# Kernel tuning notes

Measured on AMD Instinct MI355X. Metric: run time of the kernel, lower is better.

Reference implementation:

```python
import jax, jax.numpy as jnp
import numpy as np

GAMMA = 0.03125  # 1/D
REG = 1e-3


def rbf_gram(X, Y, gamma):
    # avoiding the naive [N, M, D] diff tensor from the torch source.
    xx = jnp.sum(X * X, axis=-1)  # [N]
    yy = jnp.sum(Y * Y, axis=-1)  # [M]
    sq = xx[:, None] + yy[None, :] - 2.0 * (X @ Y.T)  # [N, M]
    sq = jnp.maximum(sq, 0.0)
    return jnp.exp(-gamma * sq)


def setup_inputs() -> dict:
    key = jax.random.key(0)
    k1, k2, k3 = jax.random.split(key, 3)
    N, M, D = 8192, 8192, 32
    X_train = jax.random.normal(k1, (N, D), dtype=jnp.float32)
    y_train = jax.random.normal(k2, (N,), dtype=jnp.float32)
    X_test = jax.random.normal(k3, (M, D), dtype=jnp.float32)
    return {"X_train": X_train, "y_train": y_train, "X_test": X_test}


def reference(X_train, y_train, X_test):
    # fit: solve (K + reg * I) alpha = y
    N = X_train.shape[0]
    K = rbf_gram(X_train, X_train, GAMMA)  # [N, N]
    A = K + REG * jnp.eye(N, dtype=K.dtype)
    alpha = jnp.linalg.solve(A, y_train[:, None])[:, 0]  # [N]
    # predict: K_test @ alpha
    K_test = rbf_gram(X_test, X_train, GAMMA)  # [M, N]
    return K_test @ alpha  # [M]
```

## Files before the change

### kernel.cpp

```cpp
#include <hip/hip_runtime.h>


#define NN 8192
#define DD 32
#define REGL 1e-3f
#define NITER 94
#define NBLK 256
#define NSL 16
#define NRB 16
#define ROWS 512
#define COLS 512
#define NC2 (-0.045084220027780106f)
#define SCF (0.3002806023f)

typedef short v8s __attribute__((ext_vector_type(8)));
typedef float v4f __attribute__((ext_vector_type(4)));

__device__ __forceinline__ float fast_exp2(float x) {
#if __has_builtin(__builtin_amdgcn_exp2f)
  return __builtin_amdgcn_exp2f(x);
#else
  float r;
  asm("v_exp_f32 %0, %1" : "=v"(r) : "v"(x));
  return r;
#endif
}

__device__ __forceinline__ float ld_f(const float* p) {
  return __hip_atomic_load(p, __ATOMIC_RELAXED, __HIP_MEMORY_SCOPE_AGENT);
}
__device__ __forceinline__ void st_f(float* p, float v) {
  __hip_atomic_store(p, v, __ATOMIC_RELAXED, __HIP_MEMORY_SCOPE_AGENT);
}
__device__ __forceinline__ double ld_d(const double* p) {
  return __hip_atomic_load(p, __ATOMIC_RELAXED, __HIP_MEMORY_SCOPE_AGENT);
}
__device__ __forceinline__ void st_d(double* p, double v) {
  __hip_atomic_store(p, v, __ATOMIC_RELAXED, __HIP_MEMORY_SCOPE_AGENT);
}

__device__ __forceinline__ ushort f2bf(float x) {
  unsigned u = __float_as_uint(x);
  return (ushort)((u + 0x7fff + ((u >> 16) & 1)) >> 16);
}
__device__ __forceinline__ float bf2f(ushort b) {
  return __uint_as_float(((unsigned)b) << 16);
}

__device__ __forceinline__ double bfly64_d(double v) {
#pragma unroll
  for (int m = 1; m < 64; m <<= 1) v += __shfl_xor(v, m, 64);
  return v;
}
__device__ __forceinline__ double wave_down_sum_d(double v) {
#pragma unroll
  for (int off = 32; off > 0; off >>= 1) v += __shfl_down(v, off, 64);
  return v;
}

__device__ __forceinline__ float gather16_pair(const float* qp, int rowpair,
                                               int e) {
  const double* qpd = (const double*)qp + (rowpair >> 1);
  float mine[8], recv[8];
#pragma unroll
  for (int k = 0; k < 8; ++k) {
    union {
      double d;
      float f[2];
    } u;
    u.d = ld_d(qpd + (size_t)(e * 8 + k) * (NN / 2));
    mine[k] = e ? u.f[1] : u.f[0];
    recv[k] = e ? u.f[0] : u.f[1];
  }
#pragma unroll
  for (int k = 0; k < 8; ++k) recv[k] = __shfl_xor(recv[k], 1, 64);
  float s = 0.f;
#pragma unroll
  for (int k = 0; k < 8; ++k) s += e ? recv[k] : mine[k];
#pragma unroll
  for (int k = 0; k < 8; ++k) s += e ? mine[k] : recv[k];
  return s;
}

__device__ __forceinline__ void gbarrier(unsigned* bar, int par) {
  __builtin_amdgcn_s_waitcnt(0);
  __syncthreads();
  if (threadIdx.x == 0) {
    unsigned* gen = bar + 272;
    unsigned* base = bar + (par << 9);
    unsigned g =
        __hip_atomic_load(gen, __ATOMIC_RELAXED, __HIP_MEMORY_SCOPE_AGENT);
    unsigned a = __hip_atomic_fetch_add(&base[(blockIdx.x >> 4) * 16], 1u,
                                        __ATOMIC_RELAXED,
                                        __HIP_MEMORY_SCOPE_AGENT);
    bool pub = false;
    if (a == 15u) {
      unsigned ra = __hip_atomic_fetch_add(base + 256, 1u, __ATOMIC_RELAXED,
                                           __HIP_MEMORY_SCOPE_AGENT);
      if (ra == 15u) {
        __hip_atomic_store(gen, g + 1u, __ATOMIC_RELAXED,
                           __HIP_MEMORY_SCOPE_AGENT);
        pub = true;
#pragma unroll
        for (int k = 0; k < 16; ++k)
          __hip_atomic_store(&base[k * 16], 0u, __ATOMIC_RELAXED,
                             __HIP_MEMORY_SCOPE_AGENT);
        __hip_atomic_store(base + 256, 0u, __ATOMIC_RELAXED,
                           __HIP_MEMORY_SCOPE_AGENT);
      }
    }
    if (!pub) {
      unsigned t = 0;
      while (__hip_atomic_load(gen, __ATOMIC_RELAXED,
                               __HIP_MEMORY_SCOPE_AGENT) == g) {
        if (t < 64)
          __builtin_amdgcn_s_sleep(1);
        else
          __builtin_amdgcn_s_sleep(8);
        if (++t > (1u << 20)) break;
      }
    }
  }
  __atomic_signal_fence(__ATOMIC_SEQ_CST);
  __syncthreads();
}

__device__ __forceinline__ void conv_frag(const float* __restrict__ X, int row,
                                          int kb, v8s& h, v8s& l) {
  const float4* rp = (const float4*)(X + (size_t)row * DD + kb);
  float4 f0 = rp[0], f1 = rp[1];
  float f[8] = {f0.x, f0.y, f0.z, f0.w, f1.x, f1.y, f1.z, f1.w};
  union {
    v8s v;
    ushort u[8];
  } H, L;
#pragma unroll
  for (int j = 0; j < 8; ++j) {
    float fs = SCF * f[j];
    ushort hb = f2bf(fs);
    H.u[j] = hb;
    L.u[j] = f2bf(fs - bf2f(hb));
  }
  h = H.v;
  l = L.v;
}


__global__ void setup_zero(unsigned* __restrict__ bar) {
  int i = blockIdx.x * 256 + threadIdx.x;
  if (i < 1024) bar[i] = 0u;
}

__global__ void row_norms(const float* __restrict__ X, float* __restrict__ xx) {
  int i = blockIdx.x * blockDim.x + threadIdx.x;
  if (i < NN) {
    const float4* row = (const float4*)(X + (size_t)i * DD);
    float s = 0.f;
#pragma unroll
    for (int k = 0; k < DD / 4; ++k) {
      float4 v = row[k];
      s += v.x * v.x + v.y * v.y + v.z * v.z + v.w * v.w;
    }
    xx[i] = NC2 * s;
  }
}

__device__ __forceinline__ void mv_compute(const v8s* ah, const v8s* al,
                                           const ushort (*Bh)[512],
                                           const ushort (*Bl)[512],
                                           const float* Wj, int lane,
                                           float racc[2][4]) {
  const int n = lane & 15;
  for (int t = 0; t < 32; ++t) {
    v8s bh = *(const v8s*)&Bh[t][lane * 8];
    v8s bl = *(const v8s*)&Bl[t][lane * 8];
    float wn = Wj[t * 16 + n];
#pragma unroll
    for (int rs = 0; rs < 2; ++rs) {
      v4f c = {0.f, 0.f, 0.f, 0.f};
      c = __builtin_amdgcn_mfma_f32_16x16x32_bf16(al[rs], bh, c, 0, 0, 0);
      c = __builtin_amdgcn_mfma_f32_16x16x32_bf16(ah[rs], bl, c, 0, 0, 0);
      c = __builtin_amdgcn_mfma_f32_16x16x32_bf16(ah[rs], bh, c, 0, 0, 0);
#pragma unroll
      for (int u = 0; u < 4; ++u)
        racc[rs][u] = fmaf(fast_exp2(c[u]), wn, racc[rs][u]);
    }
  }
}


__global__ __launch_bounds__(1024, 4) void cg_persist(
    const float* __restrict__ Xtr, const float* __restrict__ Xte,
    const float* __restrict__ xx_tr, const float* __restrict__ xx_te,
    const float* __restrict__ y, float* __restrict__ qp0,
    float* __restrict__ qp1, double* __restrict__ rho_s,
    double* __restrict__ mu_s, unsigned* __restrict__ bar,
    float* __restrict__ out, int db) {
  __shared__ __align__(16) ushort Bh[32][512];
  __shared__ __align__(16) ushort Bl[32][512];
  __shared__ float Wj[512];
  __shared__ float Ebj[512];
  __shared__ float Erow[512];
  __shared__ float Rrow[512], Qrow[512];
  __shared__ float Rcol[512], Qcol[512], Pcol[512], Xcol[512];
  __shared__ double sredq[16];
  __shared__ double sredr[16];
  __shared__ float s_ab[2];

  const int tid = threadIdx.x;
  const int lane = tid & 63;
  const int wid = tid >> 6;
  const int n = lane & 15, q4 = lane >> 4;
  const int rbi = blockIdx.x & 15;
  const int sli = blockIdx.x >> 4;
  const int rowbase = rbi * ROWS;
  const int i0 = rowbase + wid * 32;
  const int jbase = sli * COLS;

#pragma unroll
  for (int rep = 0; rep < 2; ++rep) {
    int idx = rep * 1024 + tid;
    int c = idx & 511;
    int g = idx >> 9;
    int j = jbase + c;
    const float4* rp = (const float4*)(Xtr + (size_t)j * DD + g * 8);
    float4 f0 = rp[0], f1 = rp[1];
    float f[8] = {f0.x, f0.y, f0.z, f0.w, f1.x, f1.y, f1.z, f1.w};
    union {
      ushort u[8];
      uint4 qq;
    } H, L;
#pragma unroll
    for (int e = 0; e < 8; ++e) {
      float fs = SCF * f[e];
      ushort hb = f2bf(fs);
      H.u[e] = hb;
      L.u[e] = f2bf(fs - bf2f(hb));
    }
    int tile = c >> 4, cl = c & 15;
    int ln = cl + 16 * g;
    *(uint4*)&Bh[tile][ln * 8] = H.qq;
    *(uint4*)&Bl[tile][ln * 8] = L.qq;
  }
  if (tid < 512) {
    Ebj[tid] = fast_exp2(xx_tr[jbase + tid]);
    Erow[tid] = fast_exp2(xx_tr[rowbase + tid]);
    Rrow[tid] = y[rowbase + tid];
    Qrow[tid] = 0.f;
    Rcol[tid] = y[jbase + tid];
    Qcol[tid] = 0.f;
    Pcol[tid] = 0.f;
    Xcol[tid] = 0.f;
  }

  v8s ah[2], al[2];
#pragma unroll
  for (int rs = 0; rs < 2; ++rs)
    conv_frag(Xtr, i0 + rs * 16 + n, q4 * 8, ah[rs], al[rs]);

  double rho_old = 1.0, alpha_old = 1.0;
  __syncthreads();

  for (int it = 0; it < NITER; ++it) {
    float* qp = (db && (it & 1)) ? qp1 : qp0;

    if (tid >= 512) {
      int ct = tid - 512;
      Wj[ct] = Rcol[ct] * Ebj[ct];
    }
    if (sli == 0) {
      float rvv = (tid < 512) ? Rrow[tid] : 0.f;
      double acc = wave_down_sum_d((double)rvv * (double)rvv);
      if (lane == 0) sredr[wid] = acc;
    }
    __syncthreads();
    if (sli == 0 && tid == 0) {
      double t = 0.0;
#pragma unroll
      for (int k3 = 0; k3 < 16; ++k3) t += sredr[k3];
      st_d(&rho_s[(size_t)it * 256 + rbi * 16], t);
    }

    float racc[2][4] = {};
    mv_compute(ah, al, Bh, Bl, Wj, lane, racc);
#pragma unroll
    for (int rs = 0; rs < 2; ++rs)
#pragma unroll
      for (int u = 0; u < 4; ++u) {
#pragma unroll
        for (int m = 1; m < 16; m <<= 1)
          racc[rs][u] += __shfl_xor(racc[rs][u], m, 64);
      }
    double cmu = 0.0;
    if (n == 0) {
#pragma unroll
      for (int rs = 0; rs < 2; ++rs)
#pragma unroll
        for (int u = 0; u < 4; ++u) {
          int lrow = wid * 32 + rs * 16 + q4 * 4 + u;
          float qc = racc[rs][u] * Erow[lrow];
          st_f(&qp[(size_t)sli * NN + rowbase + lrow], qc);
          cmu += (double)qc * (double)Rrow[lrow];
        }
    }
    cmu = bfly64_d(cmu);
    if (lane == 0) sredq[wid] = cmu;
    __syncthreads();
    if (tid == 0) {
      double t = 0.0;
#pragma unroll
      for (int k3 = 0; k3 < 16; ++k3) t += sredq[k3];
      st_d(&mu_s[(size_t)it * 256 + blockIdx.x], t);
    }

    gbarrier(bar, db ? (it & 1) : 0);

    if (wid == 0) {
      const double* mb = mu_s + (size_t)it * 256;
      double m = ld_d(mb + lane) + ld_d(mb + lane + 64) +
                 ld_d(mb + lane + 128) + ld_d(mb + lane + 192);
      double rv_l =
          (lane < 16) ? ld_d(rho_s + (size_t)it * 256 + lane * 16) : 0.0;
      double m1 = bfly64_d(m);
      double r1 = bfly64_d(rv_l);
      double mu = m1 + (double)REGL * r1;
      double beta_d = (it == 0) ? 0.0 : r1 / rho_old;
      double alpha_d =
          (it == 0) ? r1 / mu : r1 / (mu - r1 * beta_d / alpha_old);
      rho_old = r1;
      alpha_old = alpha_d;
      if (lane == 0) {
        s_ab[0] = (float)alpha_d;
        s_ab[1] = (float)beta_d;
      }
    }
    __syncthreads();
    const float alpha = s_ab[0], beta = s_ab[1];

    if (tid < 512) {
      float s = gather16_pair(qp, rowbase + (tid & ~1), tid & 1);
      float wr = fmaf(REGL, Rrow[tid], s);
      float qn = fmaf(beta, Qrow[tid], wr);
      Qrow[tid] = qn;
      Rrow[tid] = fmaf(-alpha, qn, Rrow[tid]);
    } else {
      int ct = tid - 512;
      float s = gather16_pair(qp, jbase + (ct & ~1), ct & 1);
      float wc = fmaf(REGL, Rcol[ct], s);
      float qn = fmaf(beta, Qcol[ct], wc);
      Qcol[ct] = qn;
      float pn = fmaf(beta, Pcol[ct], Rcol[ct]);
      Pcol[ct] = pn;
      Xcol[ct] = fmaf(alpha, pn, Xcol[ct]);
      Rcol[ct] = fmaf(-alpha, qn, Rcol[ct]);
    }
    if (!db) gbarrier(bar, 1);
  }

  {
    v8s th[2], tl[2];
#pragma unroll
    for (int rs = 0; rs < 2; ++rs)
      conv_frag(Xte, i0 + rs * 16 + n, q4 * 8, th[rs], tl[rs]);
    if (tid >= 512) {
      int ct = tid - 512;
      Wj[ct] = Xcol[ct] * Ebj[ct];
    } else {
      Erow[tid] = fast_exp2(xx_te[rowbase + tid]);
    }
    __syncthreads();
    float racc[2][4] = {};
    mv_compute(th, tl, Bh, Bl, Wj, lane, racc);
#pragma unroll
    for (int rs = 0; rs < 2; ++rs)
#pragma unroll
      for (int u = 0; u < 4; ++u) {
#pragma unroll
        for (int m = 1; m < 16; m <<= 1)
          racc[rs][u] += __shfl_xor(racc[rs][u], m, 64);
      }
    if (n == 0) {
#pragma unroll
      for (int rs = 0; rs < 2; ++rs)
#pragma unroll
        for (int u = 0; u < 4; ++u) {
          int lrow = wid * 32 + rs * 16 + q4 * 4 + u;
          st_f(&qp0[(size_t)sli * NN + rowbase + lrow],
               racc[rs][u] * Erow[lrow]);
        }
    }
    gbarrier(bar, 0);
    if (sli == 0 && tid < 512) {
      const float* qb = qp0 + rowbase + tid;
      float s = 0.f;
#pragma unroll
      for (int s2 = 0; s2 < NSL; ++s2) s += ld_f(qb + (size_t)s2 * NN);
      out[rowbase + tid] = s;
    }
  }
}


extern "C" void kernel_launch(void* const* d_in, const int* in_sizes, int n_in,
                              void* d_out, int out_size, void* d_ws,
                              size_t ws_size, hipStream_t stream) {
  const float* X_train = (const float*)d_in[0];
  const float* y_train = (const float*)d_in[1];
  const float* X_test = (const float*)d_in[2];
  float* out = (float*)d_out;

  char* w = (char*)d_ws;
  size_t off = 0;
  float* xx_tr = (float*)(w + off); off += NN * 4;
  float* xx_te = (float*)(w + off); off += NN * 4;
  double* rho_s = (double*)(w + off); off += (size_t)NITER * 256 * 8;
  double* mu_s = (double*)(w + off); off += (size_t)NITER * 256 * 8;
  unsigned* bar = (unsigned*)(w + off); off += 4096;
  off = (off + 255) & ~(size_t)255;
  float* qp0 = (float*)(w + off); off += (size_t)NSL * NN * 4;
  size_t need0 = off;
  float* qp1 = (float*)(w + off); off += (size_t)NSL * NN * 4;
  size_t need1 = off;

  int db = (ws_size >= need1) ? 1 : 0;
  if (ws_size < need0) return;
  if (!db) qp1 = qp0;

  setup_zero<<<4, 256, 0, stream>>>(bar);
  row_norms<<<NN / 256, 256, 0, stream>>>(X_train, xx_tr);
  row_norms<<<NN / 256, 256, 0, stream>>>(X_test, xx_te);

  cg_persist<<<NBLK, 1024, 0, stream>>>(X_train, X_test, xx_tr, xx_te,
                                        y_train, qp0, qp1, rho_s, mu_s, bar,
                                        out, db);
}
```

Measured before the change: 1.711 ms.

## Fold CG scalar reductions into the hierarchical grid barrier via atomics

Moves the per-iteration mu and rho reductions into the grid barrier. Each block atomically adds its partial into a group slot, group leaders forward the sums to a root slot, and the last arriver computes alpha and beta once and publishes them as a packed word before bumping the generation. This replaces the post-barrier step in which every block read 256 mu partials and 16 rho partials from global memory and redid the scalar math, shortening the serial critical path of each CG iteration. It adds double-precision atomics and waitcnt fences inside the barrier, which makes the summation order nondeterministic and raises ordering subtlety.

```diff
diff --git a/kernel.cpp b/kernel.cpp
--- a/kernel.cpp
+++ b/kernel.cpp
@@ -82,22 +82,76 @@
   return s;
 }
 
-__device__ __forceinline__ void gbarrier(unsigned* bar, int par) {
+__device__ __forceinline__ void gbar_fold(unsigned* bar, int par, int scal,
+                                          double mu_p, double rho_p,
+                                          int addrho, float* s_ab) {
   __builtin_amdgcn_s_waitcnt(0);
   __syncthreads();
   if (threadIdx.x == 0) {
     unsigned* gen = bar + 272;
+    unsigned long long* abp = (unsigned long long*)(bar + 274);
+    double* st_rho = (double*)(bar + 276);
+    double* st_alp = (double*)(bar + 278);
     unsigned* base = bar + (par << 9);
+    double* gmu = (double*)(base + (blockIdx.x >> 4) * 16 + 2);
+    double* grho = (double*)(base + (blockIdx.x >> 4) * 16 + 4);
+    double* rmu = (double*)(base + 258);
+    double* rrho = (double*)(base + 260);
     unsigned g =
         __hip_atomic_load(gen, __ATOMIC_RELAXED, __HIP_MEMORY_SCOPE_AGENT);
+    if (scal) {
+      __hip_atomic_fetch_add(gmu, mu_p, __ATOMIC_RELAXED,
+                             __HIP_MEMORY_SCOPE_AGENT);
+      if (addrho)
+        __hip_atomic_fetch_add(grho, rho_p, __ATOMIC_RELAXED,
+                               __HIP_MEMORY_SCOPE_AGENT);
+      __atomic_signal_fence(__ATOMIC_SEQ_CST);
+      __builtin_amdgcn_s_waitcnt(0);
+      __atomic_signal_fence(__ATOMIC_SEQ_CST);
+    }
     unsigned a = __hip_atomic_fetch_add(&base[(blockIdx.x >> 4) * 16], 1u,
                                         __ATOMIC_RELAXED,
                                         __HIP_MEMORY_SCOPE_AGENT);
     bool pub = false;
+    float af = 0.f, bf = 0.f;
+    bool have = false;
     if (a == 15u) {
+      if (scal) {
+        double gm = ld_d(gmu), gr = ld_d(grho);
+        __hip_atomic_fetch_add(rmu, gm, __ATOMIC_RELAXED,
+                               __HIP_MEMORY_SCOPE_AGENT);
+        if (gr != 0.0)
+          __hip_atomic_fetch_add(rrho, gr, __ATOMIC_RELAXED,
+                                 __HIP_MEMORY_SCOPE_AGENT);
+        __atomic_signal_fence(__ATOMIC_SEQ_CST);
+        __builtin_amdgcn_s_waitcnt(0);
+        __atomic_signal_fence(__ATOMIC_SEQ_CST);
+      }
       unsigned ra = __hip_atomic_fetch_add(base + 256, 1u, __ATOMIC_RELAXED,
                                            __HIP_MEMORY_SCOPE_AGENT);
       if (ra == 15u) {
+        if (scal) {
+          double m1 = ld_d(rmu), r1 = ld_d(rrho);
+          double mu = m1 + (double)REGL * r1;
+          bool first = (g == 0u);
+          double rho_old = ld_d(st_rho), alpha_old = ld_d(st_alp);
+          double beta_d = first ? 0.0 : r1 / rho_old;
+          double alpha_d =
+              first ? r1 / mu : r1 / (mu - r1 * beta_d / alpha_old);
+          st_d(st_rho, r1);
+          st_d(st_alp, alpha_d);
+          af = (float)alpha_d;
+          bf = (float)beta_d;
+          have = true;
+          unsigned long long pk =
+              ((unsigned long long)__float_as_uint(bf) << 32) |
+              (unsigned long long)__float_as_uint(af);
+          __hip_atomic_store(abp, pk, __ATOMIC_RELAXED,
+                             __HIP_MEMORY_SCOPE_AGENT);
+        }
+        __atomic_signal_fence(__ATOMIC_SEQ_CST);
+        __builtin_amdgcn_s_waitcnt(0);
+        __atomic_signal_fence(__ATOMIC_SEQ_CST);
         __hip_atomic_store(gen, g + 1u, __ATOMIC_RELAXED,
                            __HIP_MEMORY_SCOPE_AGENT);
         pub = true;
@@ -107,6 +161,15 @@
                              __HIP_MEMORY_SCOPE_AGENT);
         __hip_atomic_store(base + 256, 0u, __ATOMIC_RELAXED,
                            __HIP_MEMORY_SCOPE_AGENT);
+        if (scal) {
+#pragma unroll
+          for (int k = 0; k < 16; ++k) {
+            st_d((double*)(base + k * 16 + 2), 0.0);
+            st_d((double*)(base + k * 16 + 4), 0.0);
+          }
+          st_d(rmu, 0.0);
+          st_d(rrho, 0.0);
+        }
       }
     }
     if (!pub) {
@@ -119,6 +182,17 @@
           __builtin_amdgcn_s_sleep(8);
         if (++t > (1u << 20)) break;
       }
+    }
+    if (scal) {
+      if (!have) {
+        __atomic_signal_fence(__ATOMIC_SEQ_CST);
+        unsigned long long pk = __hip_atomic_load(abp, __ATOMIC_RELAXED,
+                                                  __HIP_MEMORY_SCOPE_AGENT);
+        af = __uint_as_float((unsigned)(pk & 0xffffffffull));
+        bf = __uint_as_float((unsigned)(pk >> 32));
+      }
+      s_ab[0] = af;
+      s_ab[1] = bf;
     }
   }
   __atomic_signal_fence(__ATOMIC_SEQ_CST);
@@ -193,8 +267,7 @@
     const float* __restrict__ Xtr, const float* __restrict__ Xte,
     const float* __restrict__ xx_tr, const float* __restrict__ xx_te,
     const float* __restrict__ y, float* __restrict__ qp0,
-    float* __restrict__ qp1, double* __restrict__ rho_s,
-    double* __restrict__ mu_s, unsigned* __restrict__ bar,
+    float* __restrict__ qp1, unsigned* __restrict__ bar,
     float* __restrict__ out, int db) {
   __shared__ __align__(16) ushort Bh[32][512];
   __shared__ __align__(16) ushort Bl[32][512];
@@ -258,7 +331,6 @@
   for (int rs = 0; rs < 2; ++rs)
     conv_frag(Xtr, i0 + rs * 16 + n, q4 * 8, ah[rs], al[rs]);
 
-  double rho_old = 1.0, alpha_old = 1.0;
   __syncthreads();
 
   for (int it = 0; it < NITER; ++it) {
@@ -268,18 +340,12 @@
       int ct = tid - 512;
       Wj[ct] = Rcol[ct] * Ebj[ct];
     }
-    if (sli == 0) {
+    if (sli == rbi) {
       float rvv = (tid < 512) ? Rrow[tid] : 0.f;
       double acc = wave_down_sum_d((double)rvv * (double)rvv);
       if (lane == 0) sredr[wid] = acc;
     }
     __syncthreads();
-    if (sli == 0 && tid == 0) {
-      double t = 0.0;
-#pragma unroll
-      for (int k3 = 0; k3 < 16; ++k3) t += sredr[k3];
-      st_d(&rho_s[(size_t)it * 256 + rbi * 16], t);
-    }
 
     float racc[2][4] = {};
     mv_compute(ah, al, Bh, Bl, Wj, lane, racc);
@@ -306,35 +372,19 @@
     cmu = bfly64_d(cmu);
     if (lane == 0) sredq[wid] = cmu;
     __syncthreads();
+
+    double mu_part = 0.0, rho_part = 0.0;
     if (tid == 0) {
-      double t = 0.0;
-#pragma unroll
-      for (int k3 = 0; k3 < 16; ++k3) t += sredq[k3];
-      st_d(&mu_s[(size_t)it * 256 + blockIdx.x], t);
-    }
-
-    gbarrier(bar, db ? (it & 1) : 0);
-
-    if (wid == 0) {
-      const double* mb = mu_s + (size_t)it * 256;
-      double m = ld_d(mb + lane) + ld_d(mb + lane + 64) +
-                 ld_d(mb + lane + 128) + ld_d(mb + lane + 192);
-      double rv_l =
-          (lane < 16) ? ld_d(rho_s + (size_t)it * 256 + lane * 16) : 0.0;
-      double m1 = bfly64_d(m);
-      double r1 = bfly64_d(rv_l);
-      double mu = m1 + (double)REGL * r1;
-      double beta_d = (it == 0) ? 0.0 : r1 / rho_old;
-      double alpha_d =
-          (it == 0) ? r1 / mu : r1 / (mu - r1 * beta_d / alpha_old);
-      rho_old = r1;
-      alpha_old = alpha_d;
-      if (lane == 0) {
-        s_ab[0] = (float)alpha_d;
-        s_ab[1] = (float)beta_d;
-      }
-    }
-    __syncthreads();
+#pragma unroll
+      for (int k3 = 0; k3 < 16; ++k3) mu_part += sredq[k3];
+      if (sli == rbi) {
+#pragma unroll
+        for (int k3 = 0; k3 < 16; ++k3) rho_part += sredr[k3];
+      }
+    }
+
+    gbar_fold(bar, db ? (it & 1) : 0, 1, mu_part, rho_part, (sli == rbi),
+              s_ab);
     const float alpha = s_ab[0], beta = s_ab[1];
 
     if (tid < 512) {
@@ -354,7 +404,7 @@
       Xcol[ct] = fmaf(alpha, pn, Xcol[ct]);
       Rcol[ct] = fmaf(-alpha, qn, Rcol[ct]);
     }
-    if (!db) gbarrier(bar, 1);
+    if (!db) gbar_fold(bar, 1, 0, 0.0, 0.0, 0, s_ab);
   }
 
   {
@@ -389,7 +439,7 @@
                racc[rs][u] * Erow[lrow]);
         }
     }
-    gbarrier(bar, 0);
+    gbar_fold(bar, 0, 0, 0.0, 0.0, 0, s_ab);
     if (sli == 0 && tid < 512) {
       const float* qb = qp0 + rowbase + tid;
       float s = 0.f;
@@ -413,8 +463,6 @@
   size_t off = 0;
   float* xx_tr = (float*)(w + off); off += NN * 4;
   float* xx_te = (float*)(w + off); off += NN * 4;
-  double* rho_s = (double*)(w + off); off += (size_t)NITER * 256 * 8;
-  double* mu_s = (double*)(w + off); off += (size_t)NITER * 256 * 8;
   unsigned* bar = (unsigned*)(w + off); off += 4096;
   off = (off + 255) & ~(size_t)255;
   float* qp0 = (float*)(w + off); off += (size_t)NSL * NN * 4;
@@ -431,6 +479,5 @@
   row_norms<<<NN / 256, 256, 0, stream>>>(X_test, xx_te);
 
   cg_persist<<<NBLK, 1024, 0, stream>>>(X_train, X_test, xx_tr, xx_te,
-                                        y_train, qp0, qp1, rho_s, mu_s, bar,
-                                        out, db);
-}
+                                        y_train, qp0, qp1, bar, out, db);
+}
```

After: 1.977 ms. +15.6%, slower.
